# Kernel tuning notes

Hardware: AMD Instinct MI355X
Metric: run time of the kernel (lower is better)

Reference implementation:

```python
import math
import jax, jax.numpy as jnp
import numpy as np

DIM = 256
GROUPS = 32
EPS = 1e-5


def setup_inputs() -> dict:
    key = jax.random.key(0)
    ks = jax.random.split(key, 6)
    b, c, h, w = 4, DIM, 64, 64
    x = jax.random.normal(ks[0], (b, c, h, w), dtype=jnp.float32)
    norm_scale = jnp.ones((c,), dtype=jnp.float32)
    norm_bias = jnp.zeros((c,), dtype=jnp.float32)
    w_qkv = jax.random.normal(ks[1], (3 * c, c), dtype=jnp.float32) / math.sqrt(c)
    w_proj = jax.random.normal(ks[2], (c, c), dtype=jnp.float32) / math.sqrt(c)
    b_proj = jnp.zeros((c,), dtype=jnp.float32)
    return {"x": x, "norm_scale": norm_scale, "norm_bias": norm_bias,
            "w_qkv": w_qkv, "w_proj": w_proj, "b_proj": b_proj}


def _group_norm(x, scale, bias):
    b, c, h, w = x.shape
    xg = x.reshape(b, GROUPS, c // GROUPS, h, w)
    mean = jnp.mean(xg, axis=(2, 3, 4), keepdims=True)
    var = jnp.var(xg, axis=(2, 3, 4), keepdims=True)
    xn = ((xg - mean) * jax.lax.rsqrt(var + EPS)).reshape(b, c, h, w)
    return xn * scale[None, :, None, None] + bias[None, :, None, None]


def reference(x, norm_scale, norm_bias, w_qkv, w_proj, b_proj):
    b, c, h, w = x.shape
    n = h * w
    xn = _group_norm(x, norm_scale, norm_bias)          # residual uses normalized x (as in source)
    xf = xn.reshape(b, c, n)                            # (b, c, n)
    qkv = jnp.einsum('oc,bcn->bon', w_qkv, xf)          # 1x1 conv == channel matmul
    q, k, v = jnp.split(qkv, 3, axis=1)                 # each (b, c, n)
    attn = jnp.einsum('bci,bcj->bij', q, k) / math.sqrt(c)
    attn = jax.nn.softmax(attn, axis=-1)                # (b, n, n)
    out = jnp.einsum('bij,bcj->bci', attn, v)           # (b, c, n)
    out = jnp.einsum('oc,bcn->bon', w_proj, out) + b_proj[None, :, None]
    return out.reshape(b, c, h, w) + xn
```

## Files before the change

kernel.cpp:

```cpp
#include <hip/hip_runtime.h>
#include <hip/hip_fp8.h>
#include <cstdint>
#include <cstddef>

typedef __bf16 bf16;
typedef __attribute__((ext_vector_type(8))) __bf16 bf16x8;
typedef __attribute__((ext_vector_type(4))) float f32x4;
typedef __attribute__((ext_vector_type(4))) unsigned short u16x4;
typedef __attribute__((ext_vector_type(8))) unsigned short u16x8;

#define DEV __device__ __forceinline__

DEV unsigned short f2bf(float f) {
    unsigned int u = __builtin_bit_cast(unsigned int, f);
    u += 0x7FFFu + ((u >> 16) & 1u);
    return (unsigned short)(u >> 16);
}

DEV float bf2f(unsigned short h) {
    unsigned int u = ((unsigned int)h) << 16;
    return __builtin_bit_cast(float, u);
}

DEV unsigned char f2e4m3(float f) {
    __hip_fp8_e4m3 t(f);
    return (unsigned char)t.__x;
}

DEV void gload16(const void* g, void* l) {
    __builtin_amdgcn_global_load_lds(
        (const __attribute__((address_space(1))) unsigned int*)g,
        (__attribute__((address_space(3))) unsigned int*)l, 16, 0, 0);
}

DEV f32x4 mfma16(bf16x8 a, bf16x8 b, f32x4 c) {
    return __builtin_amdgcn_mfma_f32_16x16x32_bf16(a, b, c, 0, 0, 0);
}

__global__ void k_wconv(const float* __restrict__ wqkv, const float* __restrict__ wproj,
                        unsigned short* __restrict__ wq, unsigned short* __restrict__ wp) {
    int i = blockIdx.x * 256 + threadIdx.x;
    if (i < 768 * 256) {
        float v = wqkv[i];
        if (i < 512 * 256) v *= 0.3002806f;
        wq[i] = f2bf(v);
    } else {
        int j = i - 768 * 256;
        wp[j] = f2bf(wproj[j]);
    }
}

__global__ __launch_bounds__(256) void k_gnstats(const float* __restrict__ x,
                                                 float* __restrict__ stats) {
    int bg = blockIdx.x;
    const float4* xp = (const float4*)(x + (size_t)bg * 32768);
    int t = threadIdx.x;
    float s = 0.f, sq = 0.f;
    #pragma unroll 4
    for (int i = 0; i < 32; ++i) {
        float4 v = xp[t + i * 256];
        s  += v.x + v.y + v.z + v.w;
        sq += v.x * v.x + v.y * v.y + v.z * v.z + v.w * v.w;
    }
    #pragma unroll
    for (int m = 1; m < 64; m <<= 1) { s += __shfl_xor(s, m); sq += __shfl_xor(sq, m); }
    __shared__ float red[8];
    int w = t >> 6;
    if ((t & 63) == 0) { red[w] = s; red[4 + w] = sq; }
    __syncthreads();
    if (t == 0) {
        s  = red[0] + red[1] + red[2] + red[3];
        sq = red[4] + red[5] + red[6] + red[7];
        float mean = s * (1.f / 32768.f);
        float var  = sq * (1.f / 32768.f) - mean * mean;
        stats[bg * 2]     = mean;
        stats[bg * 2 + 1] = rsqrtf(var + 1e-5f);
    }
}

__global__ __launch_bounds__(256) void k_gnapply(const float* __restrict__ x,
        const float* __restrict__ scale, const float* __restrict__ bias,
        const float* __restrict__ stats, float* __restrict__ xn,
        unsigned short* __restrict__ xnT) {
    __shared__ __align__(16) unsigned short tsm[64][72];
    int t = threadIdx.x;
    int nb = blockIdx.x * 64, cb = blockIdx.y * 64, b = blockIdx.z;
    int cl = t >> 2, nc = (t & 3) * 16;
    int cg = cb + cl;
    float mean = stats[(b * 32 + (cg >> 3)) * 2];
    float rstd = stats[(b * 32 + (cg >> 3)) * 2 + 1];
    float sc = scale[cg] * rstd;
    float bi = bias[cg] - mean * sc;
    const float4* xrow = (const float4*)(x  + ((size_t)(b * 256 + cg)) * 4096 + nb + nc);
    float4*      orow  = (float4*)      (xn + ((size_t)(b * 256 + cg)) * 4096 + nb + nc);
    #pragma unroll
    for (int j = 0; j < 4; ++j) {
        float4 v = xrow[j];
        v.x = v.x * sc + bi; v.y = v.y * sc + bi; v.z = v.z * sc + bi; v.w = v.w * sc + bi;
        orow[j] = v;
        u16x4 us;
        us[0] = f2bf(v.x); us[1] = f2bf(v.y); us[2] = f2bf(v.z); us[3] = f2bf(v.w);
        *(u16x4*)&tsm[cl][nc + j * 4] = us;
    }
    __syncthreads();
    int nl = t >> 2, cc = (t & 3) * 16;
    u16x8 o0, o1;
    #pragma unroll
    for (int j = 0; j < 8; ++j) { o0[j] = tsm[cc + j][nl]; o1[j] = tsm[cc + 8 + j][nl]; }
    unsigned short* dst = xnT + ((size_t)(b * 4096 + nb + nl)) * 256 + cb + cc;
    *(u16x8*)dst = o0;
    *(u16x8*)(dst + 8) = o1;
}

__global__ __launch_bounds__(256) void k_qkv(const unsigned short* __restrict__ xnT,
        const unsigned short* __restrict__ wq, unsigned short* __restrict__ qkvT,
        unsigned char* __restrict__ qk8) {
    __shared__ __align__(16) char smem[65536];
    char* Asm = smem;
    char* Bsm = smem + 32768;
    int t = threadIdx.x, l = t & 63, w = t >> 6;
    int mb = blockIdx.x * 64, nb = blockIdx.y * 64;
    #pragma unroll
    for (int i = 0; i < 8; ++i) {
        int idx = (w * 8 + i) * 64 + l;
        int r = idx >> 5, p = idx & 31;
        gload16(xnT + (size_t)(mb + r) * 256 + ((p ^ (r & 7)) * 8), Asm + (w * 8 + i) * 1024);
    }
    #pragma unroll
    for (int i = 0; i < 8; ++i) {
        int idx = (w * 8 + i) * 64 + l;
        int r = idx >> 5, p = idx & 31;
        gload16(wq + (size_t)(nb + r) * 256 + ((p ^ (r & 7)) * 8), Bsm + (w * 8 + i) * 1024);
    }
    __syncthreads();
    int arow = w * 16 + (l & 15);
    bf16x8 af[8];
    #pragma unroll
    for (int ks = 0; ks < 8; ++ks)
        af[ks] = *(const bf16x8*)(Asm + arow * 512 + (((ks * 4 + (l >> 4)) ^ (arow & 7)) << 4));
    f32x4 acc[4];
    #pragma unroll
    for (int i = 0; i < 4; ++i) acc[i] = f32x4{0.f, 0.f, 0.f, 0.f};
    #pragma unroll
    for (int sub = 0; sub < 4; ++sub) {
        int brow = sub * 16 + (l & 15);
        #pragma unroll
        for (int ks = 0; ks < 8; ++ks) {
            bf16x8 bb = *(const bf16x8*)(Bsm + brow * 512 + (((ks * 4 + (l >> 4)) ^ (brow & 7)) << 4));
            acc[sub] = mfma16(af[ks], bb, acc[sub]);
        }
    }
    int row0 = mb + w * 16 + (l >> 4) * 4;
    if (nb < 512) {
        #pragma unroll
        for (int sub = 0; sub < 4; ++sub) {
            #pragma unroll
            for (int r = 0; r < 4; ++r)
                qk8[(size_t)(row0 + r) * 512 + nb + sub * 16 + (l & 15)] = f2e4m3(acc[sub][r]);
        }
    } else {
        #pragma unroll
        for (int sub = 0; sub < 4; ++sub) {
            #pragma unroll
            for (int r = 0; r < 4; ++r)
                qkvT[(size_t)(row0 + r) * 768 + nb + sub * 16 + (l & 15)] = f2bf(acc[sub][r]);
        }
    }
}

__global__ __launch_bounds__(256) void k_vtrans(const unsigned short* __restrict__ qkvT,
                                                unsigned short* __restrict__ vT) {
    __shared__ __align__(16) unsigned short tsm[64][72];
    int t = threadIdx.x;
    int nb = blockIdx.x * 64, cb = blockIdx.y * 64, b = blockIdx.z;
    int nl = t >> 2, cc = (t & 3) * 16;
    const unsigned short* src = qkvT + (size_t)(b * 4096 + nb + nl) * 768 + 512 + cb + cc;
    u16x8 v0 = *(const u16x8*)src;
    u16x8 v1 = *(const u16x8*)(src + 8);
    *(u16x8*)&tsm[nl][cc] = v0;
    *(u16x8*)&tsm[nl][cc + 8] = v1;
    __syncthreads();
    int clc = t >> 2, nn = (t & 3) * 16;
    u16x8 o0, o1;
    #pragma unroll
    for (int j = 0; j < 8; ++j) { o0[j] = tsm[nn + j][clc]; o1[j] = tsm[nn + 8 + j][clc]; }
    unsigned short* dst = vT + (size_t)(b * 256 + cb + clc) * 4096 + nb + nn;
    *(u16x8*)dst = o0;
    *(u16x8*)(dst + 8) = o1;
}

struct AttnState {
    f32x4 acc[16];
    f32x4 accSum;
    float m_run[4];
};

DEV void attn_compute(const char* Ksm, const char* Vsm, char* Psm,
                      const long long qf8[8], AttnState& st, int l) {
    f32x4 s[4];
    __builtin_amdgcn_s_setprio(1);
    #pragma unroll
    for (int jt = 0; jt < 4; ++jt) {
        f32x4 a = f32x4{0.f, 0.f, 0.f, 0.f};
        int jr = jt * 16 + (l & 15);
        #pragma unroll
        for (int ks = 0; ks < 8; ++ks) {
            int c8 = ks * 4 + (l >> 4);
            long long kb = *(const long long*)(Ksm + jr * 256 +
                            (((c8 >> 1) ^ (jr & 7)) << 4) + (c8 & 1) * 8);
            a = __builtin_amdgcn_mfma_f32_16x16x32_fp8_fp8(qf8[ks], kb, a, 0, 0, 0);
        }
        s[jt] = a;
    }
    __builtin_amdgcn_s_setprio(0);

    float tm[4];
    #pragma unroll
    for (int r = 0; r < 4; ++r) {
        float v = fmaxf(fmaxf(s[0][r], s[1][r]), fmaxf(s[2][r], s[3][r]));
        #pragma unroll
        for (int mm = 1; mm < 16; mm <<= 1) v = fmaxf(v, __shfl_xor(v, mm));
        tm[r] = v;
    }
    int defer = 1;
    #pragma unroll
    for (int r = 0; r < 4; ++r) defer &= (tm[r] <= st.m_run[r] + 8.f) ? 1 : 0;
    bool alldef = __all(defer);
    if (!alldef) {
        float sf[4];
        #pragma unroll
        for (int r = 0; r < 4; ++r) {
            float mn = fmaxf(st.m_run[r], tm[r]);
            sf[r] = __builtin_amdgcn_exp2f(st.m_run[r] - mn);
            st.m_run[r] = mn;
        }
        #pragma unroll
        for (int i = 0; i < 16; ++i) {
            st.acc[i][0] *= sf[0]; st.acc[i][1] *= sf[1];
            st.acc[i][2] *= sf[2]; st.acc[i][3] *= sf[3];
        }
        st.accSum[0] *= sf[0]; st.accSum[1] *= sf[1];
        st.accSum[2] *= sf[2]; st.accSum[3] *= sf[3];
    }

    #pragma unroll
    for (int jt = 0; jt < 4; ++jt) {
        #pragma unroll
        for (int r = 0; r < 4; ++r) {
            float pv = __builtin_amdgcn_exp2f(s[jt][r] - st.m_run[r]);
            int row = (l >> 4) * 4 + r;
            int j = jt * 16 + (l & 15);
            int byteoff = row * 128 + (((j >> 3) ^ (row & 7)) << 4) + (j & 7) * 2;
            *(unsigned short*)(Psm + byteoff) = f2bf(pv);
        }
    }
    asm volatile("s_waitcnt lgkmcnt(0)" ::: "memory");
    __builtin_amdgcn_sched_barrier(0);

    bf16x8 onesv;
    #pragma unroll
    for (int j = 0; j < 8; ++j) onesv[j] = (__bf16)1.0f;
    __builtin_amdgcn_s_setprio(1);
    #pragma unroll
    for (int js = 0; js < 2; ++js) {
        int pr = l & 15;
        bf16x8 pa = *(const bf16x8*)(Psm + pr * 128 + (((js * 4 + (l >> 4)) ^ (pr & 7)) << 4));
        #pragma unroll
        for (int sub = 0; sub < 16; ++sub) {
            int cr = sub * 16 + (l & 15);
            bf16x8 vb = *(const bf16x8*)(Vsm + cr * 128 + (((js * 4 + (l >> 4)) ^ (cr & 7)) << 4));
            st.acc[sub] = mfma16(pa, vb, st.acc[sub]);
        }
        st.accSum = mfma16(pa, onesv, st.accSum);
    }
    __builtin_amdgcn_s_setprio(0);
}

#define ATTN_STAGE(KN, VN, kvn)                                                   \
    do {                                                                          \
        _Pragma("unroll")                                                         \
        for (int i_ = 0; i_ < 2; ++i_) {              \
            int e_ = (w * 2 + i_) * 64 + l;                                       \
            int r_ = e_ >> 4, p_ = e_ & 15;                                       \
            gload16(kg8 + (size_t)((kvn) + r_) * 512 + ((p_ ^ (r_ & 7)) * 16),    \
                    (KN) + (w * 2 + i_) * 1024);                                  \
        }                                                                         \
        _Pragma("unroll")                                                         \
        for (int i_ = 0; i_ < 4; ++i_) {                        \
            int e_ = (w * 4 + i_) * 64 + l;                                       \
            int r_ = e_ >> 3, p_ = e_ & 7;                                        \
            gload16(vg0 + (size_t)r_ * 4096 + (kvn) + ((p_ ^ (r_ & 7)) * 8),      \
                    (VN) + (w * 4 + i_) * 1024);                                  \
        }                                                                         \
    } while (0)

__global__ __launch_bounds__(512, 2) void k_attn(const unsigned char* __restrict__ qk8,
        const unsigned short* __restrict__ vT, unsigned short* __restrict__ Opart,
        float* __restrict__ ml) {
    __shared__ __align__(16) char smem[114688];
    char* Ksm0 = smem;
    char* Vsm0 = smem + 16384;
    char* Ksm1 = smem + 49152;
    char* Vsm1 = smem + 65536;
    int t = threadIdx.x, l = t & 63, w = t >> 6;
    char* Psm = smem + 98304 + w * 2048;
    int bid = blockIdx.x;
    int combo = bid & 7;
    int b = combo >> 1;
    int half = combo & 1;
    int qb = (bid >> 3) * 128;
    int kv0 = half * 2048;

    const unsigned char* qrow8 = qk8 + (size_t)(b * 4096 + qb + w * 16 + (l & 15)) * 512;
    long long qf8[8];
    #pragma unroll
    for (int ks = 0; ks < 8; ++ks)
        qf8[ks] = *(const long long*)(qrow8 + ks * 32 + (l >> 4) * 8);

    AttnState st;
    #pragma unroll
    for (int i = 0; i < 16; ++i) st.acc[i] = f32x4{0.f, 0.f, 0.f, 0.f};
    st.accSum = f32x4{0.f, 0.f, 0.f, 0.f};
    #pragma unroll
    for (int r = 0; r < 4; ++r) st.m_run[r] = -3.0e38f;

    const unsigned char* kg8 = qk8 + (size_t)(b * 4096) * 512 + 256;
    const unsigned short* vg0 = vT + (size_t)(b * 256) * 4096;

    ATTN_STAGE(Ksm0, Vsm0, kv0);
    __syncthreads();

    for (int kv = kv0; kv < kv0 + 2048; kv += 128) {
        ATTN_STAGE(Ksm1, Vsm1, kv + 64);
        attn_compute(Ksm0, Vsm0, Psm, qf8, st, l);
        __syncthreads();
        int kvn2 = (kv + 128 < kv0 + 2048) ? (kv + 128) : kv0;
        ATTN_STAGE(Ksm0, Vsm0, kvn2);
        attn_compute(Ksm1, Vsm1, Psm, qf8, st, l);
        __syncthreads();
    }

    float inv[4];
    #pragma unroll
    for (int r = 0; r < 4; ++r) inv[r] = 1.f / st.accSum[r];
    unsigned short* orow = Opart + (size_t)half * 16384 * 256 +
                           (size_t)(b * 4096 + qb + w * 16) * 256;
    #pragma unroll
    for (int sub = 0; sub < 16; ++sub) {
        #pragma unroll
        for (int r = 0; r < 4; ++r)
            orow[(size_t)((l >> 4) * 4 + r) * 256 + sub * 16 + (l & 15)] = f2bf(st.acc[sub][r] * inv[r]);
    }
    if ((l & 15) == 0) {
        size_t mlbase = (size_t)(b * 4096 + qb + w * 16 + (l >> 4) * 4) * 4;
        #pragma unroll
        for (int r = 0; r < 4; ++r) {
            ml[mlbase + (size_t)r * 4 + half * 2]     = st.m_run[r];
            ml[mlbase + (size_t)r * 4 + half * 2 + 1] = st.accSum[r];
        }
    }
}

__global__ __launch_bounds__(256) void k_combine(const unsigned short* __restrict__ Opart,
        const float* __restrict__ ml, unsigned short* __restrict__ Ot) {
    int gid = blockIdx.x * 256 + threadIdx.x;
    int row = gid >> 5;
    int c0 = (gid & 31) * 8;
    float m1 = ml[row * 4], l1 = ml[row * 4 + 1];
    float m2 = ml[row * 4 + 2], l2 = ml[row * 4 + 3];
    float m = fmaxf(m1, m2);
    float a1 = __builtin_amdgcn_exp2f(m1 - m) * l1;
    float a2 = __builtin_amdgcn_exp2f(m2 - m) * l2;
    float inv = 1.f / (a1 + a2);
    float w1 = a1 * inv, w2 = a2 * inv;
    size_t off = (size_t)row * 256 + c0;
    u16x8 o1 = *(const u16x8*)(Opart + off);
    u16x8 o2 = *(const u16x8*)(Opart + (size_t)16384 * 256 + off);
    u16x8 o;
    #pragma unroll
    for (int j = 0; j < 8; ++j) o[j] = f2bf(w1 * bf2f(o1[j]) + w2 * bf2f(o2[j]));
    *(u16x8*)(Ot + off) = o;
}

__global__ __launch_bounds__(256) void k_proj(const unsigned short* __restrict__ Ot,
        const unsigned short* __restrict__ wp, const float* __restrict__ bproj,
        const float* __restrict__ xn, float* __restrict__ out) {
    __shared__ __align__(16) char smem[65536];
    char* Asm = smem;
    char* Bsm = smem + 32768;
    int t = threadIdx.x, l = t & 63, w = t >> 6;
    int mb = blockIdx.x * 64, nb = blockIdx.y * 64;
    #pragma unroll
    for (int i = 0; i < 8; ++i) {
        int idx = (w * 8 + i) * 64 + l;
        int r = idx >> 5, p = idx & 31;
        gload16(Ot + (size_t)(mb + r) * 256 + ((p ^ (r & 7)) * 8), Asm + (w * 8 + i) * 1024);
    }
    #pragma unroll
    for (int i = 0; i < 8; ++i) {
        int idx = (w * 8 + i) * 64 + l;
        int r = idx >> 5, p = idx & 31;
        gload16(wp + (size_t)(nb + r) * 256 + ((p ^ (r & 7)) * 8), Bsm + (w * 8 + i) * 1024);
    }
    __syncthreads();
    int arow = w * 16 + (l & 15);
    bf16x8 af[8];
    #pragma unroll
    for (int ks = 0; ks < 8; ++ks)
        af[ks] = *(const bf16x8*)(Asm + arow * 512 + (((ks * 4 + (l >> 4)) ^ (arow & 7)) << 4));
    f32x4 acc[4];
    #pragma unroll
    for (int i = 0; i < 4; ++i) acc[i] = f32x4{0.f, 0.f, 0.f, 0.f};
    #pragma unroll
    for (int sub = 0; sub < 4; ++sub) {
        int brow = sub * 16 + (l & 15);
        #pragma unroll
        for (int ks = 0; ks < 8; ++ks) {
            bf16x8 bb = *(const bf16x8*)(Bsm + brow * 512 + (((ks * 4 + (l >> 4)) ^ (brow & 7)) << 4));
            acc[sub] = mfma16(af[ks], bb, acc[sub]);
        }
    }
    __syncthreads();
    float* tr = (float*)smem;
    #pragma unroll
    for (int sub = 0; sub < 4; ++sub) {
        int o = sub * 16 + (l & 15);
        *(f32x4*)(tr + o * 68 + w * 16 + (l >> 4) * 4) = acc[sub];
    }
    __syncthreads();
    int b = mb >> 12;
    int nloc = mb & 4095;
    #pragma unroll
    for (int it = 0; it < 4; ++it) {
        int e = it * 256 + t;
        int o = e >> 4, m4 = (e & 15) * 4;
        f32x4 v = *(const f32x4*)(tr + o * 68 + m4);
        float bv = bproj[nb + o];
        size_t off = ((size_t)(b * 256 + nb + o)) * 4096 + nloc + m4;
        float4 xx = *(const float4*)(xn + off);
        float4 ov;
        ov.x = v[0] + bv + xx.x;
        ov.y = v[1] + bv + xx.y;
        ov.z = v[2] + bv + xx.z;
        ov.w = v[3] + bv + xx.w;
        *(float4*)(out + off) = ov;
    }
}

extern "C" void kernel_launch(void* const* d_in, const int* in_sizes, int n_in,
                              void* d_out, int out_size, void* d_ws, size_t ws_size,
                              hipStream_t stream) {
    const float* x      = (const float*)d_in[0];
    const float* nscale = (const float*)d_in[1];
    const float* nbias  = (const float*)d_in[2];
    const float* wqkv   = (const float*)d_in[3];
    const float* wproj  = (const float*)d_in[4];
    const float* bproj  = (const float*)d_in[5];
    float* out = (float*)d_out;

    char* ws = (char*)d_ws;
    float* stats = (float*)ws;
    float* xn    = (float*)(ws + 4096);
    unsigned short* xnT = (unsigned short*)(ws + 4096 + 16777216);
    unsigned short* wq  = xnT + 4194304;
    unsigned short* wp  = wq + 768 * 256;
    unsigned short* qkvT = wp + 256 * 256;
    unsigned short* vT   = qkvT + (size_t)16384 * 768;
    float* ml = (float*)(vT + (size_t)4 * 256 * 4096);
    unsigned char* qk8 = (unsigned char*)(ml + 65536);
    unsigned short* Opart = qkvT;
    unsigned short* Ot   = xnT;

    hipLaunchKernelGGL(k_wconv,   dim3(1024),       dim3(256), 0, stream, wqkv, wproj, wq, wp);
    hipLaunchKernelGGL(k_gnstats, dim3(128),        dim3(256), 0, stream, x, stats);
    hipLaunchKernelGGL(k_gnapply, dim3(64, 4, 4),   dim3(256), 0, stream, x, nscale, nbias, stats, xn, xnT);
    hipLaunchKernelGGL(k_qkv,     dim3(256, 12),    dim3(256), 0, stream, xnT, wq, qkvT, qk8);
    hipLaunchKernelGGL(k_vtrans,  dim3(64, 4, 4),   dim3(256), 0, stream, qkvT, vT);
    hipLaunchKernelGGL(k_attn,    dim3(256),        dim3(512), 0, stream, qk8, vT, Opart, ml);
    hipLaunchKernelGGL(k_combine, dim3(2048),       dim3(256), 0, stream, Opart, ml, Ot);
    hipLaunchKernelGGL(k_proj,    dim3(256, 4),     dim3(256), 0, stream, Ot, wp, bproj, xn, out);
}
```

Measured before the change: 151.3 us.

## Quantize V and P to FP8 and use FP8 MFMA for PV product

Result: slower. 156.1 us (+3.1%).

```diff
diff --git a/kernel.cpp b/kernel.cpp
--- a/kernel.cpp
+++ b/kernel.cpp
@@ -8,6 +8,7 @@
 typedef __attribute__((ext_vector_type(4))) float f32x4;
 typedef __attribute__((ext_vector_type(4))) unsigned short u16x4;
 typedef __attribute__((ext_vector_type(8))) unsigned short u16x8;
+typedef __attribute__((ext_vector_type(16))) unsigned char u8x16;
 
 #define DEV __device__ __forceinline__
 
@@ -169,7 +170,7 @@
 }
 
 __global__ __launch_bounds__(256) void k_vtrans(const unsigned short* __restrict__ qkvT,
-                                                unsigned short* __restrict__ vT) {
+                                                unsigned char* __restrict__ vT8) {
     __shared__ __align__(16) unsigned short tsm[64][72];
     int t = threadIdx.x;
     int nb = blockIdx.x * 64, cb = blockIdx.y * 64, b = blockIdx.z;
@@ -181,12 +182,14 @@
     *(u16x8*)&tsm[nl][cc + 8] = v1;
     __syncthreads();
     int clc = t >> 2, nn = (t & 3) * 16;
-    u16x8 o0, o1;
-    #pragma unroll
-    for (int j = 0; j < 8; ++j) { o0[j] = tsm[nn + j][clc]; o1[j] = tsm[nn + 8 + j][clc]; }
-    unsigned short* dst = vT + (size_t)(b * 256 + cb + clc) * 4096 + nb + nn;
-    *(u16x8*)dst = o0;
-    *(u16x8*)(dst + 8) = o1;
+    u8x16 ob;
+    #pragma unroll
+    for (int j = 0; j < 8; ++j) {
+        ob[j]     = f2e4m3(bf2f(tsm[nn + j][clc]));
+        ob[8 + j] = f2e4m3(bf2f(tsm[nn + 8 + j][clc]));
+    }
+    unsigned char* dst = vT8 + (size_t)(b * 256 + cb + clc) * 4096 + nb + nn;
+    *(u8x16*)dst = ob;
 }
 
 struct AttnState {
@@ -250,28 +253,30 @@
             float pv = __builtin_amdgcn_exp2f(s[jt][r] - st.m_run[r]);
             int row = (l >> 4) * 4 + r;
             int j = jt * 16 + (l & 15);
-            int byteoff = row * 128 + (((j >> 3) ^ (row & 7)) << 4) + (j & 7) * 2;
-            *(unsigned short*)(Psm + byteoff) = f2bf(pv);
+            int bo = (row >> 1) * 128 + (row & 1) * 64 +
+                     (((j >> 4) ^ ((row >> 1) & 3)) << 4) + (j & 15);
+            *(unsigned char*)(Psm + bo) = f2e4m3(pv);
         }
     }
     asm volatile("s_waitcnt lgkmcnt(0)" ::: "memory");
     __builtin_amdgcn_sched_barrier(0);
 
-    bf16x8 onesv;
-    #pragma unroll
-    for (int j = 0; j < 8; ++j) onesv[j] = (__bf16)1.0f;
+    const long long ones8 = 0x3838383838383838LL;
     __builtin_amdgcn_s_setprio(1);
     #pragma unroll
     for (int js = 0; js < 2; ++js) {
         int pr = l & 15;
-        bf16x8 pa = *(const bf16x8*)(Psm + pr * 128 + (((js * 4 + (l >> 4)) ^ (pr & 7)) << 4));
+        int cg = js * 4 + (l >> 4);
+        long long pa = *(const long long*)(Psm + (pr >> 1) * 128 + (pr & 1) * 64 +
+                        (((cg >> 1) ^ ((pr >> 1) & 3)) << 4) + (cg & 1) * 8);
         #pragma unroll
         for (int sub = 0; sub < 16; ++sub) {
             int cr = sub * 16 + (l & 15);
-            bf16x8 vb = *(const bf16x8*)(Vsm + cr * 128 + (((js * 4 + (l >> 4)) ^ (cr & 7)) << 4));
-            st.acc[sub] = mfma16(pa, vb, st.acc[sub]);
-        }
-        st.accSum = mfma16(pa, onesv, st.accSum);
+            long long vb = *(const long long*)(Vsm + (cr >> 1) * 128 + (cr & 1) * 64 +
+                            (((cg >> 1) ^ ((cr >> 1) & 3)) << 4) + (cg & 1) * 8);
+            st.acc[sub] = __builtin_amdgcn_mfma_f32_16x16x32_fp8_fp8(pa, vb, st.acc[sub], 0, 0, 0);
+        }
+        st.accSum = __builtin_amdgcn_mfma_f32_16x16x32_fp8_fp8(pa, ones8, st.accSum, 0, 0, 0);
     }
     __builtin_amdgcn_s_setprio(0);
 }
@@ -286,24 +291,25 @@
                     (KN) + (w * 2 + i_) * 1024);                                  \
         }                                                                         \
         _Pragma("unroll")                                                         \
-        for (int i_ = 0; i_ < 4; ++i_) {                        \
-            int e_ = (w * 4 + i_) * 64 + l;                                       \
-            int r_ = e_ >> 3, p_ = e_ & 7;                                        \
-            gload16(vg0 + (size_t)r_ * 4096 + (kvn) + ((p_ ^ (r_ & 7)) * 8),      \
-                    (VN) + (w * 4 + i_) * 1024);                                  \
+        for (int i_ = 0; i_ < 2; ++i_) {             \
+            int e_ = (w * 2 + i_) * 64 + l;                                       \
+            int c_ = ((e_ >> 3) << 1) + ((e_ >> 2) & 1);                          \
+            int pg_ = (e_ & 3) ^ ((e_ >> 3) & 3);                                 \
+            gload16(vg8 + (size_t)c_ * 4096 + (kvn) + pg_ * 16,                   \
+                    (VN) + (w * 2 + i_) * 1024);                                  \
         }                                                                         \
     } while (0)
 
 __global__ __launch_bounds__(512, 2) void k_attn(const unsigned char* __restrict__ qk8,
-        const unsigned short* __restrict__ vT, unsigned short* __restrict__ Opart,
+        const unsigned char* __restrict__ vT8, unsigned short* __restrict__ Opart,
         float* __restrict__ ml) {
-    __shared__ __align__(16) char smem[114688];
+    __shared__ __align__(16) char smem[73728];
     char* Ksm0 = smem;
     char* Vsm0 = smem + 16384;
-    char* Ksm1 = smem + 49152;
-    char* Vsm1 = smem + 65536;
+    char* Ksm1 = smem + 32768;
+    char* Vsm1 = smem + 49152;
     int t = threadIdx.x, l = t & 63, w = t >> 6;
-    char* Psm = smem + 98304 + w * 2048;
+    char* Psm = smem + 65536 + w * 1024;
     int bid = blockIdx.x;
     int combo = bid & 7;
     int b = combo >> 1;
@@ -325,7 +331,7 @@
     for (int r = 0; r < 4; ++r) st.m_run[r] = -3.0e38f;
 
     const unsigned char* kg8 = qk8 + (size_t)(b * 4096) * 512 + 256;
-    const unsigned short* vg0 = vT + (size_t)(b * 256) * 4096;
+    const unsigned char* vg8 = vT8 + (size_t)(b * 256) * 4096;
 
     ATTN_STAGE(Ksm0, Vsm0, kv0);
     __syncthreads();
@@ -465,8 +471,8 @@
     unsigned short* wq  = xnT + 4194304;
     unsigned short* wp  = wq + 768 * 256;
     unsigned short* qkvT = wp + 256 * 256;
-    unsigned short* vT   = qkvT + (size_t)16384 * 768;
-    float* ml = (float*)(vT + (size_t)4 * 256 * 4096);
+    unsigned char* vT8 = (unsigned char*)(qkvT + (size_t)16384 * 768);
+    float* ml = (float*)(vT8 + (size_t)4 * 256 * 4096);
     unsigned char* qk8 = (unsigned char*)(ml + 65536);
     unsigned short* Opart = qkvT;
     unsigned short* Ot   = xnT;
@@ -475,8 +481,8 @@
     hipLaunchKernelGGL(k_gnstats, dim3(128),        dim3(256), 0, stream, x, stats);
     hipLaunchKernelGGL(k_gnapply, dim3(64, 4, 4),   dim3(256), 0, stream, x, nscale, nbias, stats, xn, xnT);
     hipLaunchKernelGGL(k_qkv,     dim3(256, 12),    dim3(256), 0, stream, xnT, wq, qkvT, qk8);
-    hipLaunchKernelGGL(k_vtrans,  dim3(64, 4, 4),   dim3(256), 0, stream, qkvT, vT);
-    hipLaunchKernelGGL(k_attn,    dim3(256),        dim3(512), 0, stream, qk8, vT, Opart, ml);
+    hipLaunchKernelGGL(k_vtrans,  dim3(64, 4, 4),   dim3(256), 0, stream, qkvT, vT8);
+    hipLaunchKernelGGL(k_attn,    dim3(256),        dim3(512), 0, stream, qk8, vT8, Opart, ml);
     hipLaunchKernelGGL(k_combine, dim3(2048),       dim3(256), 0, stream, Opart, ml, Ot);
     hipLaunchKernelGGL(k_proj,    dim3(256, 4),     dim3(256), 0, stream, Ot, wp, bproj, xn, out);
 }
```

## Fuse V transpose into QKV GEMM and split-combine into projection load

Applied to the files above, without the earlier changes.

New measurement: 145.6 us. -3.8%, faster.

```diff
diff --git a/kernel.cpp b/kernel.cpp
--- a/kernel.cpp
+++ b/kernel.cpp
@@ -113,8 +113,8 @@
 }
 
 __global__ __launch_bounds__(256) void k_qkv(const unsigned short* __restrict__ xnT,
-        const unsigned short* __restrict__ wq, unsigned short* __restrict__ qkvT,
-        unsigned char* __restrict__ qk8) {
+        const unsigned short* __restrict__ wq, unsigned char* __restrict__ qk8,
+        unsigned short* __restrict__ vT) {
     __shared__ __align__(16) char smem[65536];
     char* Asm = smem;
     char* Bsm = smem + 32768;
@@ -159,34 +159,27 @@
                 qk8[(size_t)(row0 + r) * 512 + nb + sub * 16 + (l & 15)] = f2e4m3(acc[sub][r]);
         }
     } else {
+        __syncthreads();
+        unsigned short (*tsm)[72] = (unsigned short (*)[72])smem;
+        int rt = w * 16 + (l >> 4) * 4;
         #pragma unroll
         for (int sub = 0; sub < 4; ++sub) {
+            int ct = sub * 16 + (l & 15);
             #pragma unroll
             for (int r = 0; r < 4; ++r)
-                qkvT[(size_t)(row0 + r) * 768 + nb + sub * 16 + (l & 15)] = f2bf(acc[sub][r]);
-        }
-    }
-}
-
-__global__ __launch_bounds__(256) void k_vtrans(const unsigned short* __restrict__ qkvT,
-                                                unsigned short* __restrict__ vT) {
-    __shared__ __align__(16) unsigned short tsm[64][72];
-    int t = threadIdx.x;
-    int nb = blockIdx.x * 64, cb = blockIdx.y * 64, b = blockIdx.z;
-    int nl = t >> 2, cc = (t & 3) * 16;
-    const unsigned short* src = qkvT + (size_t)(b * 4096 + nb + nl) * 768 + 512 + cb + cc;
-    u16x8 v0 = *(const u16x8*)src;
-    u16x8 v1 = *(const u16x8*)(src + 8);
-    *(u16x8*)&tsm[nl][cc] = v0;
-    *(u16x8*)&tsm[nl][cc + 8] = v1;
-    __syncthreads();
-    int clc = t >> 2, nn = (t & 3) * 16;
-    u16x8 o0, o1;
-    #pragma unroll
-    for (int j = 0; j < 8; ++j) { o0[j] = tsm[nn + j][clc]; o1[j] = tsm[nn + 8 + j][clc]; }
-    unsigned short* dst = vT + (size_t)(b * 256 + cb + clc) * 4096 + nb + nn;
-    *(u16x8*)dst = o0;
-    *(u16x8*)(dst + 8) = o1;
+                tsm[rt + r][ct] = f2bf(acc[sub][r]);
+        }
+        __syncthreads();
+        int clc = t >> 2, nn = (t & 3) * 16;
+        u16x8 o0, o1;
+        #pragma unroll
+        for (int j = 0; j < 8; ++j) { o0[j] = tsm[nn + j][clc]; o1[j] = tsm[nn + 8 + j][clc]; }
+        int b = mb >> 12;
+        int nloc = mb & 4095;
+        unsigned short* dst = vT + (size_t)(b * 256 + (nb - 512) + clc) * 4096 + nloc + nn;
+        *(u16x8*)dst = o0;
+        *(u16x8*)(dst + 8) = o1;
+    }
 }
 
 struct AttnState {
@@ -361,30 +354,10 @@
     }
 }
 
-__global__ __launch_bounds__(256) void k_combine(const unsigned short* __restrict__ Opart,
-        const float* __restrict__ ml, unsigned short* __restrict__ Ot) {
-    int gid = blockIdx.x * 256 + threadIdx.x;
-    int row = gid >> 5;
-    int c0 = (gid & 31) * 8;
-    float m1 = ml[row * 4], l1 = ml[row * 4 + 1];
-    float m2 = ml[row * 4 + 2], l2 = ml[row * 4 + 3];
-    float m = fmaxf(m1, m2);
-    float a1 = __builtin_amdgcn_exp2f(m1 - m) * l1;
-    float a2 = __builtin_amdgcn_exp2f(m2 - m) * l2;
-    float inv = 1.f / (a1 + a2);
-    float w1 = a1 * inv, w2 = a2 * inv;
-    size_t off = (size_t)row * 256 + c0;
-    u16x8 o1 = *(const u16x8*)(Opart + off);
-    u16x8 o2 = *(const u16x8*)(Opart + (size_t)16384 * 256 + off);
-    u16x8 o;
-    #pragma unroll
-    for (int j = 0; j < 8; ++j) o[j] = f2bf(w1 * bf2f(o1[j]) + w2 * bf2f(o2[j]));
-    *(u16x8*)(Ot + off) = o;
-}
-
-__global__ __launch_bounds__(256) void k_proj(const unsigned short* __restrict__ Ot,
-        const unsigned short* __restrict__ wp, const float* __restrict__ bproj,
-        const float* __restrict__ xn, float* __restrict__ out) {
+__global__ __launch_bounds__(256) void k_proj(const unsigned short* __restrict__ Opart,
+        const float* __restrict__ ml, const unsigned short* __restrict__ wp,
+        const float* __restrict__ bproj, const float* __restrict__ xn,
+        float* __restrict__ out) {
     __shared__ __align__(16) char smem[65536];
     char* Asm = smem;
     char* Bsm = smem + 32768;
@@ -394,7 +367,20 @@
     for (int i = 0; i < 8; ++i) {
         int idx = (w * 8 + i) * 64 + l;
         int r = idx >> 5, p = idx & 31;
-        gload16(Ot + (size_t)(mb + r) * 256 + ((p ^ (r & 7)) * 8), Asm + (w * 8 + i) * 1024);
+        size_t grow = (size_t)(mb + r);
+        const u16x8* o1p = (const u16x8*)(Opart + grow * 256 + ((p ^ (r & 7)) * 8));
+        const u16x8* o2p = (const u16x8*)((const unsigned short*)o1p + (size_t)16384 * 256);
+        float m1 = ml[grow * 4],     l1 = ml[grow * 4 + 1];
+        float m2 = ml[grow * 4 + 2], l2 = ml[grow * 4 + 3];
+        float m = fmaxf(m1, m2);
+        float a1 = __builtin_amdgcn_exp2f(m1 - m) * l1;
+        float a2 = __builtin_amdgcn_exp2f(m2 - m) * l2;
+        float zinv = 1.f / (a1 + a2);
+        float w1 = a1 * zinv, w2 = a2 * zinv;
+        u16x8 o1 = *o1p, o2 = *o2p, a;
+        #pragma unroll
+        for (int j = 0; j < 8; ++j) a[j] = f2bf(w1 * bf2f(o1[j]) + w2 * bf2f(o2[j]));
+        *(u16x8*)(Asm + (w * 8 + i) * 1024 + l * 16) = a;
     }
     #pragma unroll
     for (int i = 0; i < 8; ++i) {
@@ -464,19 +450,15 @@
     unsigned short* xnT = (unsigned short*)(ws + 4096 + 16777216);
     unsigned short* wq  = xnT + 4194304;
     unsigned short* wp  = wq + 768 * 256;
-    unsigned short* qkvT = wp + 256 * 256;
-    unsigned short* vT   = qkvT + (size_t)16384 * 768;
+    unsigned short* vT  = wp + 256 * 256;
     float* ml = (float*)(vT + (size_t)4 * 256 * 4096);
     unsigned char* qk8 = (unsigned char*)(ml + 65536);
-    unsigned short* Opart = qkvT;
-    unsigned short* Ot   = xnT;
+    unsigned short* Opart = (unsigned short*)(qk8 + (size_t)16384 * 512);
 
     hipLaunchKernelGGL(k_wconv,   dim3(1024),       dim3(256), 0, stream, wqkv, wproj, wq, wp);
     hipLaunchKernelGGL(k_gnstats, dim3(128),        dim3(256), 0, stream, x, stats);
     hipLaunchKernelGGL(k_gnapply, dim3(64, 4, 4),   dim3(256), 0, stream, x, nscale, nbias, stats, xn, xnT);
-    hipLaunchKernelGGL(k_qkv,     dim3(256, 12),    dim3(256), 0, stream, xnT, wq, qkvT, qk8);
-    hipLaunchKernelGGL(k_vtrans,  dim3(64, 4, 4),   dim3(256), 0, stream, qkvT, vT);
+    hipLaunchKernelGGL(k_qkv,     dim3(256, 12),    dim3(256), 0, stream, xnT, wq, qk8, vT);
     hipLaunchKernelGGL(k_attn,    dim3(256),        dim3(512), 0, stream, qk8, vT, Opart, ml);
-    hipLaunchKernelGGL(k_combine, dim3(2048),       dim3(256), 0, stream, Opart, ml, Ot);
-    hipLaunchKernelGGL(k_proj,    dim3(256, 4),     dim3(256), 0, stream, Ot, wp, bproj, xn, out);
-}
+    hipLaunchKernelGGL(k_proj,    dim3(256, 4),     dim3(256), 0, stream, Opart, ml, wp, bproj, xn, out);
+}
```
